# Optimization experiments

Measured on AMD Instinct MI355X. Metric: run time of the kernel, lower is better.

Reference implementation:

```python
import jax, jax.numpy as jnp
import numpy as np

MARGIN = 1.0


def setup_inputs() -> dict:
    key = jax.random.key(0)
    k1, k2, k3 = jax.random.split(key, 3)
    n, d = 8192, 128
    feat1 = jax.random.normal(k1, (n, d), dtype=jnp.float32)
    feat2 = jax.random.normal(k2, (n, d), dtype=jnp.float32)
    # similarity labels in {+1, -1}, as expected by HingeEmbeddingLoss
    simi = (2 * jax.random.randint(k3, (n, n), 0, 2) - 1).astype(jnp.int32)
    return {"feat1": feat1, "feat2": feat2, "simi": simi}


def reference(feat1, feat2, simi):
    # logits[i,j] = -||feat1_i - feat2_j||^2, computed without the O(n*m*d) expand
    sq1 = jnp.sum(feat1 * feat1, axis=-1, keepdims=True)          # [n, 1]
    sq2 = jnp.sum(feat2 * feat2, axis=-1)                          # [m]
    cross = jnp.einsum('nd,md->nm', feat1, feat2)                  # [n, m]
    logits = -(sq1 + sq2[None, :] - 2.0 * cross)                   # [n, m]
    probs = jax.nn.softmax(logits, axis=1)                         # [n, m]
    # HingeEmbeddingLoss: x if y==1 else max(0, margin - x); mean reduction
    loss = jnp.where(simi == 1, probs, jnp.maximum(0.0, MARGIN - probs))
    return jnp.mean(loss)
```

## Files before the change

### kernel.cpp

```cpp
#include <hip/hip_runtime.h>
#include <hip/hip_bf16.h>
#include <stdint.h>

#define N 8192
#define D 128
#define NCHUNK 16
#define CHUNK (N / NCHUNK)
#define RT 64
#define CT 64
#define NTILES (CHUNK / CT)

typedef short bf16x8 __attribute__((ext_vector_type(8)));
typedef float f32x4 __attribute__((ext_vector_type(4)));
typedef unsigned int uint32;

#define OFF_ACC   0u
#define OFF_SQ2   1024u
#define OFF_M     40960u
#define OFF_L     (OFF_M + NCHUNK * N * 4u)
#define OFF_S     (OFF_L + NCHUNK * N * 4u)
#define OFF_F1    (OFF_S + NCHUNK * N * 4u)
#define OFF_F2    (OFF_F1 + N * D * 2u)

__global__ __launch_bounds__(256)
void prep_kernel(const float* __restrict__ f1, const float* __restrict__ f2,
                 unsigned short* __restrict__ f1b, unsigned short* __restrict__ f2b,
                 float* __restrict__ sq2) {
    const int w    = blockIdx.x * 4 + (threadIdx.x >> 6);
    const int lane = threadIdx.x & 63;
    for (int row = w; row < N; row += 1024) {
        float a0 = f1[row * D + lane];
        float a1 = f1[row * D + 64 + lane];
        float b0 = f2[row * D + lane];
        float b1 = f2[row * D + 64 + lane];
        __hip_bfloat16 t;
        t = __float2bfloat16(a0); f1b[row * D + lane]      = *(unsigned short*)&t;
        t = __float2bfloat16(a1); f1b[row * D + 64 + lane] = *(unsigned short*)&t;
        t = __float2bfloat16(b0); f2b[row * D + lane]      = *(unsigned short*)&t;
        t = __float2bfloat16(b1); f2b[row * D + 64 + lane] = *(unsigned short*)&t;
        float ss = b0 * b0 + b1 * b1;
        #pragma unroll
        for (int off = 32; off > 0; off >>= 1) ss += __shfl_xor(ss, off);
        if (lane == 0) sq2[row] = ss;
    }
}

__global__ __launch_bounds__(256)
void main_kernel(const unsigned short* __restrict__ f1b,
                 const unsigned short* __restrict__ f2b,
                 const float* __restrict__ sq2,
                 const int* __restrict__ simi,
                 float* __restrict__ pm, float* __restrict__ pl, float* __restrict__ ps,
                 uint32* __restrict__ cnt_acc) {
    __shared__ unsigned short ldsB[CT * D];
    __shared__ float ldsSq[CHUNK];

    const int tid  = threadIdx.x;
    const int wave = tid >> 6;
    const int lane = tid & 63;
    const int lo   = lane & 15;
    const int hi   = lane >> 4;

    const int rowtile = blockIdx.x;
    const int chunk   = blockIdx.y;
    const int rbase   = rowtile * RT + wave * 16;
    const int cbase0  = chunk * CHUNK;

    for (int i = tid; i < CHUNK; i += 256) ldsSq[i] = sq2[cbase0 + i];

    bf16x8 afrag[4];
    {
        const unsigned short* ap = f1b + (rbase + lo) * D + hi * 8;
        #pragma unroll
        for (int kk = 0; kk < 4; kk++)
            afrag[kk] = *reinterpret_cast<const bf16x8*>(ap + kk * 32);
    }

    const int sq_ = (tid >> 4);
    const int sg_ = tid & 15;

    const int* simi_p = simi + (size_t)(rbase + hi * 4) * N + cbase0 + 4 * lo;

    float m[4], l[4], s[4];
    #pragma unroll
    for (int r = 0; r < 4; r++) { m[r] = -1e30f; l[r] = 0.f; s[r] = 0.f; }
    uint32 cnt = 0;

    for (int t = 0; t < NTILES; t++) {
        const int cbase = cbase0 + t * CT;

        uint32 mb[4];
        #pragma unroll
        for (int r = 0; r < 4; r++) {
            int4 mk = *reinterpret_cast<const int4*>(simi_p + (size_t)r * N);
            mb[r] = (uint32)(mk.x == 1) | ((uint32)(mk.y == 1) << 1) |
                    ((uint32)(mk.z == 1) << 2) | ((uint32)(mk.w == 1) << 3);
            cnt += 4u - __popc(mb[r]);
        }

        __syncthreads();
        #pragma unroll
        for (int it = 0; it < 4; it++) {
            int q = it * 16 + sq_;
            int c = 4 * (q & 15) + (q >> 4);
            const uint4 v = *reinterpret_cast<const uint4*>(f2b + (size_t)(cbase + c) * D + sg_ * 8);
            *reinterpret_cast<uint4*>(ldsB + q * D + ((sg_ ^ (q & 15)) * 8)) = v;
        }
        __syncthreads();

        f32x4 acc[4];
        #pragma unroll
        for (int cf = 0; cf < 4; cf++) {
            acc[cf] = (f32x4){0.f, 0.f, 0.f, 0.f};
            const int brow = cf * 16 + lo;
            #pragma unroll
            for (int kk = 0; kk < 4; kk++) {
                int g = kk * 4 + hi;
                bf16x8 b = *reinterpret_cast<const bf16x8*>(
                    ldsB + brow * D + ((g ^ (brow & 15)) * 8));
                acc[cf] = __builtin_amdgcn_mfma_f32_16x16x32_bf16(afrag[kk], b, acc[cf], 0, 0, 0);
            }
        }

        f32x4 sqv = *reinterpret_cast<const f32x4*>(&ldsSq[t * CT + 4 * lo]);
        #pragma unroll
        for (int cf = 0; cf < 4; cf++)
            #pragma unroll
            for (int r = 0; r < 4; r++)
                acc[cf][r] = 2.0f * acc[cf][r] - sqv[cf];

        #pragma unroll
        for (int r = 0; r < 4; r++) {
            float tm = fmaxf(fmaxf(acc[0][r], acc[1][r]), fmaxf(acc[2][r], acc[3][r]));
            #pragma unroll
            for (int off = 1; off < 16; off <<= 1)
                tm = fmaxf(tm, __shfl_xor(tm, off));
            float mn = fmaxf(m[r], tm);
            float al = __expf(m[r] - mn);
            l[r] *= al; s[r] *= al; m[r] = mn;
        }
        #pragma unroll
        for (int r = 0; r < 4; r++)
            #pragma unroll
            for (int cf = 0; cf < 4; cf++) {
                float p = __expf(acc[cf][r] - m[r]);
                l[r] += p;
                if ((mb[r] >> cf) & 1u) s[r] += p;
            }
        simi_p += CT;
    }

    #pragma unroll
    for (int r = 0; r < 4; r++) {
        #pragma unroll
        for (int off = 1; off < 16; off <<= 1) {
            l[r] += __shfl_xor(l[r], off);
            s[r] += __shfl_xor(s[r], off);
        }
    }
    if (lo == 0) {
        #pragma unroll
        for (int r = 0; r < 4; r++) {
            int row = rbase + hi * 4 + r;
            int idx = chunk * N + row;
            pm[idx] = m[r]; pl[idx] = l[r]; ps[idx] = s[r];
        }
    }
    #pragma unroll
    for (int off = 1; off < 64; off <<= 1) cnt += __shfl_xor(cnt, off);
    if (lane == 0) atomicAdd(cnt_acc, cnt);
}

__global__ void merge_kernel(const float* __restrict__ pm, const float* __restrict__ pl,
                             const float* __restrict__ ps, float* __restrict__ s_acc) {
    const int row = blockIdx.x * 256 + threadIdx.x;
    float M = -1e30f;
    #pragma unroll
    for (int k = 0; k < NCHUNK; k++) M = fmaxf(M, pm[k * N + row]);
    float L = 0.f, S = 0.f;
    #pragma unroll
    for (int k = 0; k < NCHUNK; k++) {
        float e = __expf(pm[k * N + row] - M);
        L += pl[k * N + row] * e;
        S += ps[k * N + row] * e;
    }
    float r = S / L;
    #pragma unroll
    for (int off = 32; off > 0; off >>= 1) r += __shfl_xor(r, off);
    __shared__ float red[4];
    int lane = threadIdx.x & 63, w = threadIdx.x >> 6;
    if (lane == 0) red[w] = r;
    __syncthreads();
    if (threadIdx.x == 0) atomicAdd(s_acc, red[0] + red[1] + red[2] + red[3]);
}

__global__ void final_kernel(const float* __restrict__ s_acc, const uint32* __restrict__ cnt_acc,
                             float* __restrict__ out) {
    double S = (double)s_acc[0];
    double C = (double)cnt_acc[0];
    double n = (double)N;
    out[0] = (float)((2.0 * S + C - n) / (n * n));
}

extern "C" void kernel_launch(void* const* d_in, const int* in_sizes, int n_in,
                              void* d_out, int out_size, void* d_ws, size_t ws_size,
                              hipStream_t stream) {
    const float* f1   = (const float*)d_in[0];
    const float* f2   = (const float*)d_in[1];
    const int*   simi = (const int*)d_in[2];
    float* out = (float*)d_out;
    char* ws = (char*)d_ws;

    float*  acc_s = (float*)(ws + OFF_ACC);
    uint32* acc_c = (uint32*)(ws + OFF_ACC + 4);
    float*  sq2   = (float*)(ws + OFF_SQ2);
    float*  pm    = (float*)(ws + OFF_M);
    float*  pl    = (float*)(ws + OFF_L);
    float*  ps    = (float*)(ws + OFF_S);
    unsigned short* f1b = (unsigned short*)(ws + OFF_F1);
    unsigned short* f2b = (unsigned short*)(ws + OFF_F2);

    hipMemsetAsync(ws + OFF_ACC, 0, 64, stream);
    prep_kernel<<<256, 256, 0, stream>>>(f1, f2, f1b, f2b, sq2);
    main_kernel<<<dim3(N / RT, NCHUNK), 256, 0, stream>>>(f1b, f2b, sq2, simi, pm, pl, ps, acc_c);
    merge_kernel<<<N / 256, 256, 0, stream>>>(pm, pl, ps, acc_s);
    final_kernel<<<1, 1, 0, stream>>>(acc_s, acc_c, out);
}
```

Before: 422.2 us.

## Pre-pack similarity labels into bitmasks and double rows per wave

Adds a pack_kernel that streams the 256MB int32 label matrix once and converts it to a bitmask via wave ballots, also counting positives. The main kernel then reads 32-bit packed masks instead of int4 labels, and each wave now handles 32 rows (RT 128) so every LDS B fragment feeds two MFMAs. The label read stays a full pass over the matrix, but it is now a separate, coalesced streaming kernel rather than strided loads interleaved with compute. This adds an extra launch and a small workspace buffer, and raises register pressure in the main kernel.

```diff
diff --git a/kernel.cpp b/kernel.cpp
--- a/kernel.cpp
+++ b/kernel.cpp
@@ -6,13 +6,14 @@
 #define D 128
 #define NCHUNK 16
 #define CHUNK (N / NCHUNK)
-#define RT 64
+#define RT 128
 #define CT 64
 #define NTILES (CHUNK / CT)
 
 typedef short bf16x8 __attribute__((ext_vector_type(8)));
 typedef float f32x4 __attribute__((ext_vector_type(4)));
 typedef unsigned int uint32;
+typedef unsigned long long uint64;
 
 #define OFF_ACC   0u
 #define OFF_SQ2   1024u
@@ -21,6 +22,7 @@
 #define OFF_S     (OFF_L + NCHUNK * N * 4u)
 #define OFF_F1    (OFF_S + NCHUNK * N * 4u)
 #define OFF_F2    (OFF_F1 + N * D * 2u)
+#define OFF_PACK  (OFF_F2 + N * D * 2u)
 
 __global__ __launch_bounds__(256)
 void prep_kernel(const float* __restrict__ f1, const float* __restrict__ f2,
@@ -46,12 +48,40 @@
 }
 
 __global__ __launch_bounds__(256)
+void pack_kernel(const int* __restrict__ simi, uint64* __restrict__ packed,
+                 uint32* __restrict__ pos_acc) {
+    const int row  = blockIdx.x;
+    const int wave = threadIdx.x >> 6;
+    const int lane = threadIdx.x & 63;
+    const int* rp = simi + (size_t)row * N;
+    uint32 pos = 0;
+    for (int seg = wave; seg < N / 256; seg += 4) {
+        const int cb = seg * 256;
+        int v0 = rp[cb + lane];
+        int v1 = rp[cb + 64 + lane];
+        int v2 = rp[cb + 128 + lane];
+        int v3 = rp[cb + 192 + lane];
+        uint64 b0 = __ballot(v0 == 1);
+        uint64 b1 = __ballot(v1 == 1);
+        uint64 b2 = __ballot(v2 == 1);
+        uint64 b3 = __ballot(v3 == 1);
+        if (lane == 0) {
+            uint64* dst = packed + (size_t)row * (N / 64) + seg * 4;
+            ulonglong2 p01 = {b0, b1}, p23 = {b2, b3};
+            *reinterpret_cast<ulonglong2*>(dst)     = p01;
+            *reinterpret_cast<ulonglong2*>(dst + 2) = p23;
+            pos += (uint32)(__popcll(b0) + __popcll(b1) + __popcll(b2) + __popcll(b3));
+        }
+    }
+    if (lane == 0 && pos) atomicAdd(pos_acc, pos);
+}
+
+__global__ __launch_bounds__(256)
 void main_kernel(const unsigned short* __restrict__ f1b,
                  const unsigned short* __restrict__ f2b,
                  const float* __restrict__ sq2,
-                 const int* __restrict__ simi,
-                 float* __restrict__ pm, float* __restrict__ pl, float* __restrict__ ps,
-                 uint32* __restrict__ cnt_acc) {
+                 const uint32* __restrict__ packed32,
+                 float* __restrict__ pm, float* __restrict__ pl, float* __restrict__ ps) {
     __shared__ unsigned short ldsB[CT * D];
     __shared__ float ldsSq[CHUNK];
 
@@ -63,40 +93,42 @@
 
     const int rowtile = blockIdx.x;
     const int chunk   = blockIdx.y;
-    const int rbase   = rowtile * RT + wave * 16;
+    const int rbase   = rowtile * RT + wave * 32;
     const int cbase0  = chunk * CHUNK;
 
     for (int i = tid; i < CHUNK; i += 256) ldsSq[i] = sq2[cbase0 + i];
 
-    bf16x8 afrag[4];
-    {
-        const unsigned short* ap = f1b + (rbase + lo) * D + hi * 8;
+    bf16x8 afrag[2][4];
+    #pragma unroll
+    for (int a = 0; a < 2; a++) {
+        const unsigned short* ap = f1b + (size_t)(rbase + a * 16 + lo) * D + hi * 8;
         #pragma unroll
         for (int kk = 0; kk < 4; kk++)
-            afrag[kk] = *reinterpret_cast<const bf16x8*>(ap + kk * 32);
+            afrag[a][kk] = *reinterpret_cast<const bf16x8*>(ap + kk * 32);
     }
 
     const int sq_ = (tid >> 4);
     const int sg_ = tid & 15;
 
-    const int* simi_p = simi + (size_t)(rbase + hi * 4) * N + cbase0 + 4 * lo;
-
-    float m[4], l[4], s[4];
-    #pragma unroll
-    for (int r = 0; r < 4; r++) { m[r] = -1e30f; l[r] = 0.f; s[r] = 0.f; }
-    uint32 cnt = 0;
+    const uint32* pk = packed32 + (size_t)(rbase + hi * 4) * (N / 32)
+                                + (cbase0 >> 5) + (lo >> 3);
+    const int mshift = 4 * (lo & 7);
+
+    float m[2][4], l[2][4], s[2][4];
+    #pragma unroll
+    for (int a = 0; a < 2; a++)
+        #pragma unroll
+        for (int r = 0; r < 4; r++) { m[a][r] = -1e30f; l[a][r] = 0.f; s[a][r] = 0.f; }
 
     for (int t = 0; t < NTILES; t++) {
         const int cbase = cbase0 + t * CT;
 
-        uint32 mb[4];
-        #pragma unroll
-        for (int r = 0; r < 4; r++) {
-            int4 mk = *reinterpret_cast<const int4*>(simi_p + (size_t)r * N);
-            mb[r] = (uint32)(mk.x == 1) | ((uint32)(mk.y == 1) << 1) |
-                    ((uint32)(mk.z == 1) << 2) | ((uint32)(mk.w == 1) << 3);
-            cnt += 4u - __popc(mb[r]);
-        }
+        uint32 mb[2][4];
+        #pragma unroll
+        for (int a = 0; a < 2; a++)
+            #pragma unroll
+            for (int r = 0; r < 4; r++)
+                mb[a][r] = (pk[(size_t)(a * 16 + r) * (N / 32)] >> mshift) & 0xfu;
 
         __syncthreads();
         #pragma unroll
@@ -108,67 +140,75 @@
         }
         __syncthreads();
 
-        f32x4 acc[4];
+        f32x4 acc[2][4];
         #pragma unroll
         for (int cf = 0; cf < 4; cf++) {
-            acc[cf] = (f32x4){0.f, 0.f, 0.f, 0.f};
+            acc[0][cf] = (f32x4){0.f, 0.f, 0.f, 0.f};
+            acc[1][cf] = (f32x4){0.f, 0.f, 0.f, 0.f};
             const int brow = cf * 16 + lo;
             #pragma unroll
             for (int kk = 0; kk < 4; kk++) {
                 int g = kk * 4 + hi;
                 bf16x8 b = *reinterpret_cast<const bf16x8*>(
                     ldsB + brow * D + ((g ^ (brow & 15)) * 8));
-                acc[cf] = __builtin_amdgcn_mfma_f32_16x16x32_bf16(afrag[kk], b, acc[cf], 0, 0, 0);
+                acc[0][cf] = __builtin_amdgcn_mfma_f32_16x16x32_bf16(afrag[0][kk], b, acc[0][cf], 0, 0, 0);
+                acc[1][cf] = __builtin_amdgcn_mfma_f32_16x16x32_bf16(afrag[1][kk], b, acc[1][cf], 0, 0, 0);
             }
         }
 
         f32x4 sqv = *reinterpret_cast<const f32x4*>(&ldsSq[t * CT + 4 * lo]);
         #pragma unroll
-        for (int cf = 0; cf < 4; cf++)
+        for (int a = 0; a < 2; a++) {
+            #pragma unroll
+            for (int cf = 0; cf < 4; cf++)
+                #pragma unroll
+                for (int r = 0; r < 4; r++)
+                    acc[a][cf][r] = 2.0f * acc[a][cf][r] - sqv[cf];
+
+            #pragma unroll
+            for (int r = 0; r < 4; r++) {
+                float tm = fmaxf(fmaxf(acc[a][0][r], acc[a][1][r]),
+                                 fmaxf(acc[a][2][r], acc[a][3][r]));
+                #pragma unroll
+                for (int off = 1; off < 16; off <<= 1)
+                    tm = fmaxf(tm, __shfl_xor(tm, off));
+                float mn = fmaxf(m[a][r], tm);
+                float al = __expf(m[a][r] - mn);
+                l[a][r] *= al; s[a][r] *= al; m[a][r] = mn;
+            }
             #pragma unroll
             for (int r = 0; r < 4; r++)
-                acc[cf][r] = 2.0f * acc[cf][r] - sqv[cf];
-
+                #pragma unroll
+                for (int cf = 0; cf < 4; cf++) {
+                    float p = __expf(acc[a][cf][r] - m[a][r]);
+                    l[a][r] += p;
+                    if ((mb[a][r] >> cf) & 1u) s[a][r] += p;
+                }
+        }
+        pk += 2;
+    }
+
+    #pragma unroll
+    for (int a = 0; a < 2; a++) {
         #pragma unroll
         for (int r = 0; r < 4; r++) {
-            float tm = fmaxf(fmaxf(acc[0][r], acc[1][r]), fmaxf(acc[2][r], acc[3][r]));
-            #pragma unroll
-            for (int off = 1; off < 16; off <<= 1)
-                tm = fmaxf(tm, __shfl_xor(tm, off));
-            float mn = fmaxf(m[r], tm);
-            float al = __expf(m[r] - mn);
-            l[r] *= al; s[r] *= al; m[r] = mn;
-        }
-        #pragma unroll
-        for (int r = 0; r < 4; r++)
-            #pragma unroll
-            for (int cf = 0; cf < 4; cf++) {
-                float p = __expf(acc[cf][r] - m[r]);
-                l[r] += p;
-                if ((mb[r] >> cf) & 1u) s[r] += p;
-            }
-        simi_p += CT;
-    }
-
-    #pragma unroll
-    for (int r = 0; r < 4; r++) {
-        #pragma unroll
-        for (int off = 1; off < 16; off <<= 1) {
-            l[r] += __shfl_xor(l[r], off);
-            s[r] += __shfl_xor(s[r], off);
+            #pragma unroll
+            for (int off = 1; off < 16; off <<= 1) {
+                l[a][r] += __shfl_xor(l[a][r], off);
+                s[a][r] += __shfl_xor(s[a][r], off);
+            }
         }
     }
     if (lo == 0) {
         #pragma unroll
-        for (int r = 0; r < 4; r++) {
-            int row = rbase + hi * 4 + r;
-            int idx = chunk * N + row;
-            pm[idx] = m[r]; pl[idx] = l[r]; ps[idx] = s[r];
-        }
-    }
-    #pragma unroll
-    for (int off = 1; off < 64; off <<= 1) cnt += __shfl_xor(cnt, off);
-    if (lane == 0) atomicAdd(cnt_acc, cnt);
+        for (int a = 0; a < 2; a++)
+            #pragma unroll
+            for (int r = 0; r < 4; r++) {
+                int row = rbase + a * 16 + hi * 4 + r;
+                int idx = chunk * N + row;
+                pm[idx] = m[a][r]; pl[idx] = l[a][r]; ps[idx] = s[a][r];
+            }
+    }
 }
 
 __global__ void merge_kernel(const float* __restrict__ pm, const float* __restrict__ pl,
@@ -194,10 +234,10 @@
     if (threadIdx.x == 0) atomicAdd(s_acc, red[0] + red[1] + red[2] + red[3]);
 }
 
-__global__ void final_kernel(const float* __restrict__ s_acc, const uint32* __restrict__ cnt_acc,
+__global__ void final_kernel(const float* __restrict__ s_acc, const uint32* __restrict__ pos_acc,
                              float* __restrict__ out) {
     double S = (double)s_acc[0];
-    double C = (double)cnt_acc[0];
+    double C = (double)N * (double)N - (double)pos_acc[0];
     double n = (double)N;
     out[0] = (float)((2.0 * S + C - n) / (n * n));
 }
@@ -211,18 +251,21 @@
     float* out = (float*)d_out;
     char* ws = (char*)d_ws;
 
-    float*  acc_s = (float*)(ws + OFF_ACC);
-    uint32* acc_c = (uint32*)(ws + OFF_ACC + 4);
-    float*  sq2   = (float*)(ws + OFF_SQ2);
-    float*  pm    = (float*)(ws + OFF_M);
-    float*  pl    = (float*)(ws + OFF_L);
-    float*  ps    = (float*)(ws + OFF_S);
+    float*  acc_s  = (float*)(ws + OFF_ACC);
+    uint32* acc_p  = (uint32*)(ws + OFF_ACC + 4);
+    float*  sq2    = (float*)(ws + OFF_SQ2);
+    float*  pm     = (float*)(ws + OFF_M);
+    float*  pl     = (float*)(ws + OFF_L);
+    float*  ps     = (float*)(ws + OFF_S);
     unsigned short* f1b = (unsigned short*)(ws + OFF_F1);
     unsigned short* f2b = (unsigned short*)(ws + OFF_F2);
+    uint64* packed = (uint64*)(ws + OFF_PACK);
 
     hipMemsetAsync(ws + OFF_ACC, 0, 64, stream);
     prep_kernel<<<256, 256, 0, stream>>>(f1, f2, f1b, f2b, sq2);
-    main_kernel<<<dim3(N / RT, NCHUNK), 256, 0, stream>>>(f1b, f2b, sq2, simi, pm, pl, ps, acc_c);
+    pack_kernel<<<N, 256, 0, stream>>>(simi, packed, acc_p);
+    main_kernel<<<dim3(N / RT, NCHUNK), 256, 0, stream>>>(f1b, f2b, sq2,
+                                                          (const uint32*)packed, pm, pl, ps);
     merge_kernel<<<N / 256, 256, 0, stream>>>(pm, pl, ps, acc_s);
-    final_kernel<<<1, 1, 0, stream>>>(acc_s, acc_c, out);
-}
+    final_kernel<<<1, 1, 0, stream>>>(acc_s, acc_p, out);
+}
```

Result: slower. 732.0 us (+73.4%).
